# Kernel tuning notes

Measured on AMD Instinct MI355X. Metric: run time of the kernel, lower is better.

Reference implementation:

```python
import jax, jax.numpy as jnp
import numpy as np

B, S, I, H, NC = 256, 1024, 64, 128, 10

def setup_inputs() -> dict:
    key = jax.random.key(0)
    ks = jax.random.split(key, 12)
    s_dh = 1.0 / np.sqrt(I)
    s_lstm = 1.0 / np.sqrt(H)
    return {
        "values": jax.random.normal(ks[0], (B, S, I), dtype=jnp.float32),
        "masks": jax.random.randint(ks[1], (B, S, I), 0, 2, dtype=jnp.int32),
        "deltas": jax.random.uniform(ks[2], (B, S, I), dtype=jnp.float32),
        "W_dh": jax.random.uniform(ks[3], (H, I), minval=-s_dh, maxval=s_dh),
        "b_dh": jax.random.uniform(ks[4], (H,), minval=-s_dh, maxval=s_dh),
        "W_dx": jax.random.uniform(ks[5], (I, I), minval=-s_dh, maxval=s_dh),
        "b_dx": jax.random.uniform(ks[6], (I,), minval=-s_dh, maxval=s_dh),
        "W_ih": jax.random.uniform(ks[7], (4 * H, 2 * I), minval=-s_lstm, maxval=s_lstm),
        "W_hh": jax.random.uniform(ks[8], (4 * H, H), minval=-s_lstm, maxval=s_lstm),
        "b_ih": jax.random.uniform(ks[9], (4 * H,), minval=-s_lstm, maxval=s_lstm),
        "b_hh": jax.random.uniform(ks[10], (4 * H,), minval=-s_lstm, maxval=s_lstm),
        "W_out": jax.random.uniform(ks[11], (NC, H), minval=-s_lstm, maxval=s_lstm),
        "b_out": jnp.zeros((NC,), dtype=jnp.float32),
    }

def _grud_forward(values, masks_f, deltas, W_dh, b_dh, W_dx, b_dx, W_ih, W_hh, b_ih, b_hh, W_out, b_out):
    eye = jnp.eye(W_dx.shape[0], dtype=W_dx.dtype)
    W_dx_diag = W_dx * eye  # TemporalDecay diag=True masks weight with identity

    def step(carry, xs):
        h, c = carry
        x, m, d = xs  # each (B, I)
        gamma_h = jnp.exp(-jax.nn.relu(d @ W_dh.T + b_dh))  # (B, H)
        gamma_x = jnp.exp(-jax.nn.relu(d @ W_dx_diag.T + b_dx))  # (B, I)
        h = h * gamma_h
        x_h = m * x + (1.0 - m) * (1.0 - gamma_x)  # forwards=None -> f = 1.0
        inp = jnp.concatenate([x_h, m], axis=1)  # (B, 2I)
        gates = inp @ W_ih.T + b_ih + h @ W_hh.T + b_hh  # (B, 4H)
        i_g, f_g, g_g, o_g = jnp.split(gates, 4, axis=1)
        c = jax.nn.sigmoid(f_g) * c + jax.nn.sigmoid(i_g) * jnp.tanh(g_g)
        h = jax.nn.sigmoid(o_g) * jnp.tanh(c)
        return (h, c), x_h

    b, _, _ = values.shape
    hdim = W_hh.shape[1]
    h0 = jnp.zeros((b, hdim), dtype=values.dtype)
    c0 = jnp.zeros((b, hdim), dtype=values.dtype)
    xs = (jnp.swapaxes(values, 0, 1), jnp.swapaxes(masks_f, 0, 1), jnp.swapaxes(deltas, 0, 1))
    (h, c), imputes = jax.lax.scan(step, (h0, c0), xs)
    impute_tensor = jnp.swapaxes(imputes, 0, 1)  # (B, S, I)
    y_h = h @ W_out.T + b_out  # dropout is identity in eval mode
    return y_h, impute_tensor

def reference(values, masks, deltas, W_dh, b_dh, W_dx, b_dx, W_ih, W_hh, b_ih, b_hh, W_out, b_out):
    masks_f = masks.astype(values.dtype)
    return _grud_forward(values, masks_f, deltas, W_dh, b_dh, W_dx, b_dx, W_ih, W_hh, b_ih, b_hh, W_out, b_out)
```

## Files before the change

kernel.cpp:

```cpp
#include <hip/hip_runtime.h>
#include <hip/hip_fp16.h>

#define NB   256
#define NS   1024
#define NI   64
#define NH   128
#define NCLS 10

typedef _Float16 h1;
typedef h1 h2 __attribute__((ext_vector_type(2)));

struct alignas(16) H8 { h2 v[4]; };

__device__ __forceinline__ h2 mk2(float a, float b) {
  h2 r; r[0] = (h1)a; r[1] = (h1)b; return r;
}

__device__ __forceinline__ float fdot2(h2 a, h2 b, float c) {
#if __has_builtin(__builtin_amdgcn_fdot2)
  return __builtin_amdgcn_fdot2(a, b, c, false);
#else
  return c + (float)a[0] * (float)b[0] + (float)a[1] * (float)b[1];
#endif
}

__device__ __forceinline__ float fast_rcp(float x) {
#if __has_builtin(__builtin_amdgcn_rcpf)
  return __builtin_amdgcn_rcpf(x);
#else
  return 1.0f / x;
#endif
}

__device__ __forceinline__ float tanh_f(float x) {
  return 2.f * fast_rcp(1.f + __expf(-2.f * x)) - 1.f;
}

__global__ __launch_bounds__(512, 1) void grud_fused(
    const float* __restrict__ values,
    const int*   __restrict__ masks,
    const float* __restrict__ deltas,
    const float* __restrict__ W_dh, const float* __restrict__ b_dh,
    const float* __restrict__ W_dx, const float* __restrict__ b_dx,
    const float* __restrict__ W_ih, const float* __restrict__ W_hh,
    const float* __restrict__ b_ih, const float* __restrict__ b_hh,
    const float* __restrict__ W_out, const float* __restrict__ b_out,
    float* __restrict__ out)
{
  const int b   = blockIdx.x;
  const int tid = threadIdx.x;
  const int l   = tid & 63;
  const int w   = tid >> 6;
  const int gt  = l & 3;
  const int j   = (w << 4) | (l >> 2);
  const int n   = (gt << 7) | j;

  __shared__ alignas(16) h2 inp_lds[2][64];
  __shared__ alignas(16) h2 h_lds[2][64];
  __shared__ float hfin[NH];

  h2 wih[64], whh[64];
  {
    const float4* a4 = reinterpret_cast<const float4*>(W_ih + (size_t)n * 128);
    const float4* c4 = reinterpret_cast<const float4*>(W_hh + (size_t)n * 128);
#pragma unroll
    for (int k = 0; k < 32; ++k) {
      float4 a = a4[k];
      wih[2*k]   = mk2(a.x, a.y);
      wih[2*k+1] = mk2(a.z, a.w);
      float4 c = c4[k];
      whh[2*k]   = mk2(c.x, c.y);
      whh[2*k+1] = mk2(c.z, c.w);
    }
  }
  float wdhf[16];
  {
    const float4* a4 = reinterpret_cast<const float4*>(W_dh + j * 64 + gt * 16);
#pragma unroll
    for (int k = 0; k < 4; ++k) {
      float4 a = a4[k];
      wdhf[4*k] = a.x; wdhf[4*k+1] = a.y; wdhf[4*k+2] = a.z; wdhf[4*k+3] = a.w;
    }
  }
  const float bias_n = b_ih[n] + b_hh[n];
  const float bdh_j  = b_dh[j];
  float wdx_i = 0.f, bdx_i = 0.f;
  if (tid < NI) { wdx_i = W_dx[tid * 64 + tid]; bdx_i = b_dx[tid]; }

  const size_t base_b = (size_t)b * NS * NI;
  float* out_y   = out;
  float* out_imp = out + NB * NCLS;

  if (tid < 64) {
    h_lds[0][tid] = mk2(0.f, 0.f);
    float x0 = values[base_b + tid];
    float m0 = (float)masks[base_b + tid];
    float d0 = deltas[base_b + tid];
    float gx = __expf(-fmaxf(d0 * wdx_i + bdx_i, 0.f));
    float xh = m0 * x0 + (1.f - m0) * (1.f - gx);
    out_imp[base_b + tid] = xh;
    h1* ip = reinterpret_cast<h1*>(&inp_lds[0][0]);
    ip[tid]      = (h1)xh;
    ip[64 + tid] = (h1)m0;
  }

  float c_st = 0.f, h_st = 0.f;
  int cur = 0;

  for (int t = 0; t < NS; ++t) {
    __syncthreads();
    const int    tn = (t + 1 < NS) ? (t + 1) : (NS - 1);
    const size_t nb = base_b + (size_t)tn * NI;

    const float4* dn4 = reinterpret_cast<const float4*>(deltas + nb + gt * 16);
    float4 pd0 = dn4[0], pd1 = dn4[1], pd2 = dn4[2], pd3 = dn4[3];
    float px = 0.f, pm = 0.f, pdv = 0.f;
    if (tid < NI) {
      px  = values[nb + tid];
      pm  = (float)masks[nb + tid];
      pdv = deltas[nb + tid];
    }

    float acc = bias_n;
#pragma unroll
    for (int k = 0; k < 16; ++k) {
      H8 iv = *reinterpret_cast<const H8*>(&inp_lds[cur][4 * k]);
      H8 hv = *reinterpret_cast<const H8*>(&h_lds[cur][4 * k]);
      acc = fdot2(iv.v[0], wih[4*k+0], acc);
      acc = fdot2(iv.v[1], wih[4*k+1], acc);
      acc = fdot2(iv.v[2], wih[4*k+2], acc);
      acc = fdot2(iv.v[3], wih[4*k+3], acc);
      acc = fdot2(hv.v[0], whh[4*k+0], acc);
      acc = fdot2(hv.v[1], whh[4*k+1], acc);
      acc = fdot2(hv.v[2], whh[4*k+2], acc);
      acc = fdot2(hv.v[3], whh[4*k+3], acc);
    }

    float um  = (gt == 2) ? (-2.f * acc) : (-acc);
    float ev  = __expf(um);
    float rv  = fast_rcp(1.f + ev);
    float act = (gt == 2) ? (2.f * rv - 1.f) : rv;

    const int qb = l & ~3;
    float ia = __shfl(act, qb + 0, 64);
    float fa = __shfl(act, qb + 1, 64);
    float ga = __shfl(act, qb + 2, 64);
    float oa = __shfl(act, qb + 3, 64);

    c_st = fa * c_st + ia * ga;
    h_st = oa * tanh_f(c_st);

    if (tid < NI) {
      float gx = __expf(-fmaxf(pdv * wdx_i + bdx_i, 0.f));
      float xh = pm * px + (1.f - pm) * (1.f - gx);
      if (t + 1 < NS) out_imp[nb + tid] = xh;
      h1* ip = reinterpret_cast<h1*>(&inp_lds[cur ^ 1][0]);
      ip[tid]      = (h1)xh;
      ip[64 + tid] = (h1)pm;
    }

    float part = pd0.x*wdhf[0]  + pd0.y*wdhf[1]  + pd0.z*wdhf[2]  + pd0.w*wdhf[3];
    part      += pd1.x*wdhf[4]  + pd1.y*wdhf[5]  + pd1.z*wdhf[6]  + pd1.w*wdhf[7];
    part      += pd2.x*wdhf[8]  + pd2.y*wdhf[9]  + pd2.z*wdhf[10] + pd2.w*wdhf[11];
    part      += pd3.x*wdhf[12] + pd3.y*wdhf[13] + pd3.z*wdhf[14] + pd3.w*wdhf[15];
    part += __shfl_xor(part, 1, 64);
    part += __shfl_xor(part, 2, 64);
    float gh = __expf(-fmaxf(part + bdh_j, 0.f));
    float hd = h_st * gh;
    if (gt == 0) reinterpret_cast<h1*>(&h_lds[cur ^ 1][0])[j] = (h1)hd;

    cur ^= 1;
  }

  if (gt == 0) hfin[j] = h_st;
  __syncthreads();
  if (tid < NCLS) {
    float acc = b_out[tid];
    const float4* wo4 = reinterpret_cast<const float4*>(W_out + tid * NH);
#pragma unroll
    for (int k = 0; k < 32; ++k) {
      float4 a = wo4[k];
      acc += a.x * hfin[4*k] + a.y * hfin[4*k+1] + a.z * hfin[4*k+2] + a.w * hfin[4*k+3];
    }
    out_y[b * NCLS + tid] = acc;
  }
}

extern "C" void kernel_launch(void* const* d_in, const int* in_sizes, int n_in,
                              void* d_out, int out_size, void* d_ws, size_t ws_size,
                              hipStream_t stream) {
  (void)in_sizes; (void)n_in; (void)d_ws; (void)ws_size; (void)out_size;
  grud_fused<<<dim3(NB), dim3(512), 0, stream>>>(
      (const float*)d_in[0],  (const int*)d_in[1],   (const float*)d_in[2],
      (const float*)d_in[3],  (const float*)d_in[4], (const float*)d_in[5],
      (const float*)d_in[6],  (const float*)d_in[7], (const float*)d_in[8],
      (const float*)d_in[9],  (const float*)d_in[10],(const float*)d_in[11],
      (const float*)d_in[12], (float*)d_out);
}
```

Measured before the change: 1.811 ms.

## Split gate dot products across 8 lanes per hidden unit with DPP reduction

```diff
diff --git a/kernel.cpp b/kernel.cpp
--- a/kernel.cpp
+++ b/kernel.cpp
@@ -9,7 +9,6 @@
 
 typedef _Float16 h1;
 typedef h1 h2 __attribute__((ext_vector_type(2)));
-
 struct alignas(16) H8 { h2 v[4]; };
 
 __device__ __forceinline__ h2 mk2(float a, float b) {
@@ -36,7 +35,23 @@
   return 2.f * fast_rcp(1.f + __expf(-2.f * x)) - 1.f;
 }
 
-__global__ __launch_bounds__(512, 1) void grud_fused(
+__device__ __forceinline__ float sigm(float x) {
+  return fast_rcp(1.f + __expf(-x));
+}
+
+template<int CTRL>
+__device__ __forceinline__ float dpp_add(float x) {
+  int y = __builtin_amdgcn_update_dpp(0, __float_as_int(x), CTRL, 0xF, 0xF, true);
+  return x + __int_as_float(y);
+}
+__device__ __forceinline__ float red8(float x) {
+  x = dpp_add<0xB1>(x);
+  x = dpp_add<0x4E>(x);
+  x = dpp_add<0x141>(x);
+  return x;
+}
+
+__global__ __launch_bounds__(1024, 4) void grud_fused(
     const float* __restrict__ values,
     const int*   __restrict__ masks,
     const float* __restrict__ deltas,
@@ -51,39 +66,45 @@
   const int tid = threadIdx.x;
   const int l   = tid & 63;
   const int w   = tid >> 6;
-  const int gt  = l & 3;
-  const int j   = (w << 4) | (l >> 2);
-  const int n   = (gt << 7) | j;
-
-  __shared__ alignas(16) h2 inp_lds[2][64];
-  __shared__ alignas(16) h2 h_lds[2][64];
+  const int q   = l & 7;
+  const int g   = l >> 3;
+  const int j   = (w << 3) | g;
+  const int e0  = q << 5;
+
+  __shared__ alignas(16) h1 opA[256];
+  __shared__ alignas(16) h1 opB[256];
   __shared__ float hfin[NH];
 
-  h2 wih[64], whh[64];
+  h2 wt0[16], wt1[16], wt2[16], wt3[16];
   {
-    const float4* a4 = reinterpret_cast<const float4*>(W_ih + (size_t)n * 128);
-    const float4* c4 = reinterpret_cast<const float4*>(W_hh + (size_t)n * 128);
-#pragma unroll
-    for (int k = 0; k < 32; ++k) {
-      float4 a = a4[k];
-      wih[2*k]   = mk2(a.x, a.y);
-      wih[2*k+1] = mk2(a.z, a.w);
-      float4 c = c4[k];
-      whh[2*k]   = mk2(c.x, c.y);
-      whh[2*k+1] = mk2(c.z, c.w);
-    }
-  }
-  float wdhf[16];
+    const size_t roff = (e0 < 128) ? (size_t)e0 : (size_t)(e0 - 128);
+    const float* wbase = (e0 < 128) ? W_ih : W_hh;
+#define LOADW(WT, R)                                                          \
+    {                                                                         \
+      const float4* w4 = reinterpret_cast<const float4*>(                     \
+          wbase + ((size_t)((R) * NH + j)) * 128 + roff);                     \
+      _Pragma("unroll")                                                       \
+      for (int k = 0; k < 8; ++k) {                                           \
+        float4 f = w4[k];                                                     \
+        WT[2 * k]     = mk2(f.x, f.y);                                        \
+        WT[2 * k + 1] = mk2(f.z, f.w);                                        \
+      }                                                                       \
+    }
+    LOADW(wt0, 0) LOADW(wt1, 1) LOADW(wt2, 2) LOADW(wt3, 3)
+#undef LOADW
+  }
+  const float bs0 = b_ih[j]            + b_hh[j];
+  const float bs1 = b_ih[NH + j]       + b_hh[NH + j];
+  const float bs2 = b_ih[2 * NH + j]   + b_hh[2 * NH + j];
+  const float bs3 = b_ih[3 * NH + j]   + b_hh[3 * NH + j];
+  h2 wd0, wd1, wd2, wd3;
   {
-    const float4* a4 = reinterpret_cast<const float4*>(W_dh + j * 64 + gt * 16);
-#pragma unroll
-    for (int k = 0; k < 4; ++k) {
-      float4 a = a4[k];
-      wdhf[4*k] = a.x; wdhf[4*k+1] = a.y; wdhf[4*k+2] = a.z; wdhf[4*k+3] = a.w;
-    }
-  }
-  const float bias_n = b_ih[n] + b_hh[n];
-  const float bdh_j  = b_dh[j];
+    const float4* a4 = reinterpret_cast<const float4*>(W_dh + j * 64 + q * 8);
+    float4 f0 = a4[0], f1 = a4[1];
+    wd0 = mk2(f0.x, f0.y); wd1 = mk2(f0.z, f0.w);
+    wd2 = mk2(f1.x, f1.y); wd3 = mk2(f1.z, f1.w);
+  }
+  const float bdh = b_dh[j];
   float wdx_i = 0.f, bdx_i = 0.f;
   if (tid < NI) { wdx_i = W_dx[tid * 64 + tid]; bdx_i = b_dx[tid]; }
 
@@ -91,29 +112,29 @@
   float* out_y   = out;
   float* out_imp = out + NB * NCLS;
 
-  if (tid < 64) {
-    h_lds[0][tid] = mk2(0.f, 0.f);
+  if (tid < NH) opA[128 + tid] = (h1)0.f;
+  if (tid < NI) {
     float x0 = values[base_b + tid];
     float m0 = (float)masks[base_b + tid];
     float d0 = deltas[base_b + tid];
     float gx = __expf(-fmaxf(d0 * wdx_i + bdx_i, 0.f));
     float xh = m0 * x0 + (1.f - m0) * (1.f - gx);
     out_imp[base_b + tid] = xh;
-    h1* ip = reinterpret_cast<h1*>(&inp_lds[0][0]);
-    ip[tid]      = (h1)xh;
-    ip[64 + tid] = (h1)m0;
-  }
-
+    opA[tid]      = (h1)xh;
+    opA[64 + tid] = (h1)m0;
+  }
+
+  h1* cur = opA;
+  h1* nxt = opB;
   float c_st = 0.f, h_st = 0.f;
-  int cur = 0;
 
   for (int t = 0; t < NS; ++t) {
     __syncthreads();
     const int    tn = (t + 1 < NS) ? (t + 1) : (NS - 1);
     const size_t nb = base_b + (size_t)tn * NI;
 
-    const float4* dn4 = reinterpret_cast<const float4*>(deltas + nb + gt * 16);
-    float4 pd0 = dn4[0], pd1 = dn4[1], pd2 = dn4[2], pd3 = dn4[3];
+    const float4* dn4 = reinterpret_cast<const float4*>(deltas + nb + q * 8);
+    float4 pa = dn4[0], pb = dn4[1];
     float px = 0.f, pm = 0.f, pdv = 0.f;
     if (tid < NI) {
       px  = values[nb + tid];
@@ -121,58 +142,71 @@
       pdv = deltas[nb + tid];
     }
 
-    float acc = bias_n;
-#pragma unroll
-    for (int k = 0; k < 16; ++k) {
-      H8 iv = *reinterpret_cast<const H8*>(&inp_lds[cur][4 * k]);
-      H8 hv = *reinterpret_cast<const H8*>(&h_lds[cur][4 * k]);
-      acc = fdot2(iv.v[0], wih[4*k+0], acc);
-      acc = fdot2(iv.v[1], wih[4*k+1], acc);
-      acc = fdot2(iv.v[2], wih[4*k+2], acc);
-      acc = fdot2(iv.v[3], wih[4*k+3], acc);
-      acc = fdot2(hv.v[0], whh[4*k+0], acc);
-      acc = fdot2(hv.v[1], whh[4*k+1], acc);
-      acc = fdot2(hv.v[2], whh[4*k+2], acc);
-      acc = fdot2(hv.v[3], whh[4*k+3], acc);
-    }
-
-    float um  = (gt == 2) ? (-2.f * acc) : (-acc);
-    float ev  = __expf(um);
-    float rv  = fast_rcp(1.f + ev);
-    float act = (gt == 2) ? (2.f * rv - 1.f) : rv;
-
-    const int qb = l & ~3;
-    float ia = __shfl(act, qb + 0, 64);
-    float fa = __shfl(act, qb + 1, 64);
-    float ga = __shfl(act, qb + 2, 64);
-    float oa = __shfl(act, qb + 3, 64);
+    const H8* s4 = reinterpret_cast<const H8*>(cur + e0);
+    H8 o0 = s4[0], o1 = s4[1], o2 = s4[2], o3 = s4[3];
+
+    float a0 = 0.f, a1 = 0.f, a2 = 0.f, a3 = 0.f;
+#pragma unroll
+    for (int p = 0; p < 4; ++p) {
+      a0 = fdot2(o0.v[p], wt0[p], a0);
+      a1 = fdot2(o0.v[p], wt1[p], a1);
+      a2 = fdot2(o0.v[p], wt2[p], a2);
+      a3 = fdot2(o0.v[p], wt3[p], a3);
+    }
+#pragma unroll
+    for (int p = 0; p < 4; ++p) {
+      a0 = fdot2(o1.v[p], wt0[4 + p], a0);
+      a1 = fdot2(o1.v[p], wt1[4 + p], a1);
+      a2 = fdot2(o1.v[p], wt2[4 + p], a2);
+      a3 = fdot2(o1.v[p], wt3[4 + p], a3);
+    }
+#pragma unroll
+    for (int p = 0; p < 4; ++p) {
+      a0 = fdot2(o2.v[p], wt0[8 + p], a0);
+      a1 = fdot2(o2.v[p], wt1[8 + p], a1);
+      a2 = fdot2(o2.v[p], wt2[8 + p], a2);
+      a3 = fdot2(o2.v[p], wt3[8 + p], a3);
+    }
+#pragma unroll
+    for (int p = 0; p < 4; ++p) {
+      a0 = fdot2(o3.v[p], wt0[12 + p], a0);
+      a1 = fdot2(o3.v[p], wt1[12 + p], a1);
+      a2 = fdot2(o3.v[p], wt2[12 + p], a2);
+      a3 = fdot2(o3.v[p], wt3[12 + p], a3);
+    }
+
+    float gi = red8(a0) + bs0;
+    float gf = red8(a1) + bs1;
+    float gg = red8(a2) + bs2;
+    float go = red8(a3) + bs3;
+
+    float ia = sigm(gi);
+    float fa = sigm(gf);
+    float ga = tanh_f(gg);
+    float oa = sigm(go);
 
     c_st = fa * c_st + ia * ga;
     h_st = oa * tanh_f(c_st);
+
+    h2 p0 = mk2(pa.x, pa.y), p1 = mk2(pa.z, pa.w);
+    h2 p2 = mk2(pb.x, pb.y), p3 = mk2(pb.z, pb.w);
+    float part = fdot2(p3, wd3, fdot2(p2, wd2, fdot2(p1, wd1, fdot2(p0, wd0, 0.f))));
+    part = red8(part);
+    float gh = __expf(-fmaxf(part + bdh, 0.f));
 
     if (tid < NI) {
       float gx = __expf(-fmaxf(pdv * wdx_i + bdx_i, 0.f));
       float xh = pm * px + (1.f - pm) * (1.f - gx);
       if (t + 1 < NS) out_imp[nb + tid] = xh;
-      h1* ip = reinterpret_cast<h1*>(&inp_lds[cur ^ 1][0]);
-      ip[tid]      = (h1)xh;
-      ip[64 + tid] = (h1)pm;
-    }
-
-    float part = pd0.x*wdhf[0]  + pd0.y*wdhf[1]  + pd0.z*wdhf[2]  + pd0.w*wdhf[3];
-    part      += pd1.x*wdhf[4]  + pd1.y*wdhf[5]  + pd1.z*wdhf[6]  + pd1.w*wdhf[7];
-    part      += pd2.x*wdhf[8]  + pd2.y*wdhf[9]  + pd2.z*wdhf[10] + pd2.w*wdhf[11];
-    part      += pd3.x*wdhf[12] + pd3.y*wdhf[13] + pd3.z*wdhf[14] + pd3.w*wdhf[15];
-    part += __shfl_xor(part, 1, 64);
-    part += __shfl_xor(part, 2, 64);
-    float gh = __expf(-fmaxf(part + bdh_j, 0.f));
-    float hd = h_st * gh;
-    if (gt == 0) reinterpret_cast<h1*>(&h_lds[cur ^ 1][0])[j] = (h1)hd;
-
-    cur ^= 1;
-  }
-
-  if (gt == 0) hfin[j] = h_st;
+      nxt[tid]      = (h1)xh;
+      nxt[64 + tid] = (h1)pm;
+    }
+    if (q == 0) nxt[128 + j] = (h1)(h_st * gh);
+
+    h1* tmp = cur; cur = nxt; nxt = tmp;
+  }
+
+  if (q == 0) hfin[j] = h_st;
   __syncthreads();
   if (tid < NCLS) {
     float acc = b_out[tid];
@@ -180,7 +214,8 @@
 #pragma unroll
     for (int k = 0; k < 32; ++k) {
       float4 a = wo4[k];
-      acc += a.x * hfin[4*k] + a.y * hfin[4*k+1] + a.z * hfin[4*k+2] + a.w * hfin[4*k+3];
+      acc += a.x * hfin[4 * k] + a.y * hfin[4 * k + 1] +
+             a.z * hfin[4 * k + 2] + a.w * hfin[4 * k + 3];
     }
     out_y[b * NCLS + tid] = acc;
   }
@@ -190,7 +225,7 @@
                               void* d_out, int out_size, void* d_ws, size_t ws_size,
                               hipStream_t stream) {
   (void)in_sizes; (void)n_in; (void)d_ws; (void)ws_size; (void)out_size;
-  grud_fused<<<dim3(NB), dim3(512), 0, stream>>>(
+  grud_fused<<<dim3(NB), dim3(1024), 0, stream>>>(
       (const float*)d_in[0],  (const int*)d_in[1],   (const float*)d_in[2],
       (const float*)d_in[3],  (const float*)d_in[4], (const float*)d_in[5],
       (const float*)d_in[6],  (const float*)d_in[7], (const float*)d_in[8],
```

New measurement: 1.503 ms. -17.0%, faster.
